# Optimization experiments

Hardware: AMD Instinct MI355X
Metric: run time of the kernel (lower is better)

The kernel has to match this reference:

```python
import jax, jax.numpy as jnp
import numpy as np
from jax import lax

INIT_STRIDE = 10.0
COARSE_STRIDE = 4.0
DOWN_SAMPLE = 4.0
NUM_POINT = 128
N_INST = 2000


def setup_inputs() -> dict:
    key = jax.random.key(0)
    ks = jax.random.split(key, 12)
    B, C, H, W = 4, 64, 256, 256
    return {
        'cnn_feature': jax.random.normal(ks[0], (B, C, H, W), jnp.float32),
        'wh_pred': jax.random.normal(ks[1], (B, NUM_POINT * 2, H, W), jnp.float32),
        'ct_ind': jax.random.randint(ks[2], (N_INST,), 0, H * W, jnp.int64 if jax.config.jax_enable_x64 else jnp.int32),
        'ct_img_idx': jax.random.randint(ks[3], (N_INST,), 0, B, jnp.int64 if jax.config.jax_enable_x64 else jnp.int32),
        'conv1_w': jax.random.normal(ks[4], (256, 64, 3, 3), jnp.float32) * 0.05,
        'conv1_b': jax.random.normal(ks[5], (256,), jnp.float32) * 0.05,
        'conv2_w': jax.random.normal(ks[6], (64, 256, 1, 1), jnp.float32) * 0.05,
        'conv2_b': jax.random.normal(ks[7], (64,), jnp.float32) * 0.05,
        'w_poly': jax.random.normal(ks[8], (NUM_POINT * 4, (NUM_POINT + 1) * 64), jnp.float32) * 0.02,
        'w_fuse': jax.random.normal(ks[9], (NUM_POINT * 2, NUM_POINT * 4), jnp.float32) * 0.02,
        'b_fuse': jax.random.normal(ks[10], (NUM_POINT * 2,), jnp.float32) * 0.02,
    }


def bilinear_sample(feat, pts, img_idx):
    # feat [B,C,H,W]; pts [N,P,2] pixel coords; img_idx [N]
    # matches torch grid_sample(align_corners=False, padding_mode='zeros')
    # with grid = pts/(WH/2) - 1  =>  sample coord = pts - 0.5
    B, C, H, W = feat.shape
    sx = pts[..., 0] - 0.5
    sy = pts[..., 1] - 0.5
    x0 = jnp.floor(sx).astype(jnp.int32); x1 = x0 + 1
    y0 = jnp.floor(sy).astype(jnp.int32); y1 = y0 + 1
    wx1 = sx - x0; wx0 = 1.0 - wx1
    wy1 = sy - y0; wy0 = 1.0 - wy1
    bidx = img_idx[:, None].astype(jnp.int32)  # [N,1]

    def corner(yc, xc, w):
        valid = (xc >= 0) & (xc < W) & (yc >= 0) & (yc < H)
        g = feat[bidx, :, jnp.clip(yc, 0, H - 1), jnp.clip(xc, 0, W - 1)]  # [N,P,C]
        return g * (w * valid)[..., None]

    out = (corner(y0, x0, wy0 * wx0) + corner(y0, x1, wy0 * wx1)
           + corner(y1, x0, wy1 * wx0) + corner(y1, x1, wy1 * wx1))
    return out  # [N,P,C]


def _forward(cnn_feature, wh_pred, ct_ind, ct_img_idx, conv1_w, conv1_b, conv2_w, conv2_b, w_poly, w_fuse, b_fuse):
    B, Cf, H, W = cnn_feature.shape
    N = ct_ind.shape[0]
    ct_x = jnp.clip(ct_ind % W, 0, W - 1)
    ct_y = jnp.clip(ct_ind // W, 0, H - 1)
    # gather polygon offsets at center locations: [N, 2*P] -> [N, P, 2]
    ct_offset = wh_pred[ct_img_idx, :, ct_y, ct_x].reshape(N, NUM_POINT, 2)
    ct = jnp.stack([ct_x, ct_y], axis=1).astype(jnp.float32)  # [N,2]
    init_polys = ct_offset * INIT_STRIDE + ct[:, None, :]  # [N,P,2]

    # Refine.trans_feature: conv3x3(64->256)+ReLU -> conv1x1(256->64)
    dn = ('NCHW', 'OIHW', 'NCHW')
    f = lax.conv_general_dilated(cnn_feature, conv1_w, (1, 1), 'SAME', dimension_numbers=dn) + conv1_b[None, :, None, None]
    f = jax.nn.relu(f)
    f = lax.conv_general_dilated(f, conv2_w, (1, 1), 'VALID', dimension_numbers=dn) + conv2_b[None, :, None, None]

    points = jnp.concatenate([ct[:, None, :], init_polys], axis=1)  # [N,P+1,2]
    fp = bilinear_sample(f, points, ct_img_idx)  # [N,P+1,64]
    fp = fp.transpose(0, 2, 1).reshape(N, -1)  # [N, 64*(P+1)] (C-major like torch)

    off = fp @ w_poly.T            # trans_poly (no bias)
    off = off @ w_fuse.T + b_fuse  # trans_fuse
    off = off.reshape(N, NUM_POINT, 2)
    coarse_polys = off * COARSE_STRIDE + lax.stop_gradient(init_polys)
    # stacked outputs: poly_init*down, poly_coarse*down -> [2,N,P,2]
    return jnp.stack([init_polys * DOWN_SAMPLE, coarse_polys * DOWN_SAMPLE])


def reference(cnn_feature, wh_pred, ct_ind, ct_img_idx, conv1_w, conv1_b, conv2_w, conv2_b, w_poly, w_fuse, b_fuse):
    return _forward(cnn_feature, wh_pred, ct_ind, ct_img_idx, conv1_w, conv1_b, conv2_w, conv2_b, w_poly, w_fuse, b_fuse)
```

## Files before the change

kernel.cpp:

```cpp
#include <hip/hip_runtime.h>

typedef unsigned short ushort_t;
typedef __bf16 bf16x8 __attribute__((ext_vector_type(8)));
typedef float f32x4 __attribute__((ext_vector_type(4)));

__device__ __forceinline__ ushort_t f2b(float f) {
  union { float f; unsigned u; } v; v.f = f;
  unsigned r = v.u + 0x7FFFu + ((v.u >> 16) & 1u);
  return (ushort_t)(r >> 16);
}
__device__ __forceinline__ float b2f(ushort_t u) {
  union { unsigned u; float f; } v; v.u = ((unsigned)u) << 16;
  return v.f;
}
__device__ __forceinline__ f32x4 MFMA(bf16x8 a, bf16x8 b, f32x4 c) {
  return __builtin_amdgcn_mfma_f32_16x16x32_bf16(a, b, c, 0, 0, 0);
}
__device__ __forceinline__ void gload_lds16(const ushort_t* g, ushort_t* l) {
  __builtin_amdgcn_global_load_lds(
      (const __attribute__((address_space(1))) unsigned int*)g,
      (__attribute__((address_space(3))) unsigned int*)l, 16, 0, 0);
}

#define XTW 258

__global__ void zero_border_kernel(ushort_t* __restrict__ xt) {
  int i = blockIdx.x * 256 + threadIdx.x;
  if (i >= 32896) return;
  int px_id = i >> 3, oct = (i & 7) << 3;
  int img = px_id / 1028, r = px_id - img * 1028;
  int row, col;
  if (r < 516) { row = (r < 258) ? 0 : 257; col = (r < 258) ? r : r - 258; }
  else { int rr = r - 516; row = 1 + (rr >> 1); col = (rr & 1) ? 257 : 0; }
  uint4 z = make_uint4(0, 0, 0, 0);
  *(uint4*)(xt + (((size_t)img * XTW + row) * XTW + col) * 64 + oct) = z;
}

__global__ void cast_xt_kernel(const float* __restrict__ x, ushort_t* __restrict__ xt) {
  __shared__ float tile[64][65];
  int blk = blockIdx.x;
  int b = blk >> 10, rest = blk & 1023;
  int y = rest >> 2, xseg = (rest & 3) << 6;
  int p0 = y * 256 + xseg;
  int t = threadIdx.x;
#pragma unroll
  for (int rep = 0; rep < 16; ++rep) {
    int lin = rep * 256 + t;
    int c = lin >> 6, p = lin & 63;
    tile[c][p] = x[((size_t)(b * 64 + c)) * 65536 + p0 + p];
  }
  __syncthreads();
#pragma unroll
  for (int rep = 0; rep < 2; ++rep) {
    int u = rep * 256 + t;
    int p = u >> 3, cc = (u & 7) << 3;
    union { ushort_t s[8]; uint4 v; } pk;
#pragma unroll
    for (int j = 0; j < 8; ++j) pk.s[j] = f2b(tile[cc + j][p]);
    int gx = xseg + p + 1;
    size_t base = (((size_t)b * XTW + (y + 1)) * XTW + gx) * 64;
    *(uint4*)(xt + base + (cc ^ ((gx & 7) << 3))) = pk.v;
  }
}

__global__ void cast_w1t_kernel(const float* __restrict__ w1, ushort_t* __restrict__ w1t2) {
  int i = blockIdx.x * 256 + threadIdx.x;
  int tap = i / 16384;
  int rem = i & 16383;
  int nn = rem >> 6, c = rem & 63;
  int g = nn >> 4, l15v = nn & 15;
  int kk = c >> 5, lg = (c >> 3) & 3, j = c & 7;
  int lanev = lg * 16 + l15v;
  w1t2[((tap * 2 + kk) * 16 + g) * 512 + lanev * 8 + j] = f2b(w1[(nn * 64 + c) * 9 + tap]);
}

__global__ void cast_f32_bf16_kernel(const float* __restrict__ src, ushort_t* __restrict__ dst, int n) {
  for (int i = blockIdx.x * blockDim.x + threadIdx.x; i < n; i += gridDim.x * blockDim.x)
    dst[i] = f2b(src[i]);
}

__global__ void cast_wp_kernel(const float* __restrict__ src, ushort_t* __restrict__ dst) {
  for (int i = blockIdx.x * blockDim.x + threadIdx.x; i < 4227072; i += gridDim.x * blockDim.x) {
    int row = i / 8256;
    int col = i - row * 8256;
    dst[row * 8256 + (col ^ ((row & 7) << 3))] = f2b(src[i]);
  }
}

__global__ void prep_kernel(const float* __restrict__ wh, const int* __restrict__ ct_ind,
                            const int* __restrict__ ct_b, float* __restrict__ out,
                            float* __restrict__ pts) {
  int n = blockIdx.x, t = threadIdx.x;
  int ci = ct_ind[n];
  int b = ct_b[n];
  int ctx = ci & 255;
  int cty = (ci >> 8) & 255;
  float fx = (float)ctx, fy = (float)cty;
  size_t base = ((size_t)b * 256 + 2 * t) * 65536 + (size_t)cty * 256 + ctx;
  float ox = wh[base];
  float oy = wh[base + 65536];
  float ix = ox * 10.f + fx, iy = oy * 10.f + fy;
  out[(n * 128 + t) * 2]     = ix * 4.f;
  out[(n * 128 + t) * 2 + 1] = iy * 4.f;
  float* pn = pts + (size_t)n * 258;
  if (t == 0) { pn[0] = fx; pn[1] = fy; }
  pn[2 + t * 2] = ix;
  pn[3 + t * 2] = iy;
}

__global__ __launch_bounds__(512, 2)
void conv_fused_kernel(const ushort_t* __restrict__ xt, const ushort_t* __restrict__ w1t2,
                       const float* __restrict__ b1, const float* __restrict__ w2,
                       const float* __restrict__ b2, ushort_t* __restrict__ f2) {
  __shared__ __align__(16) char smem[163840];
  ushort_t* strip = (ushort_t*)smem;
  ushort_t* F1    = (ushort_t*)smem;
  ushort_t* W2l   = (ushort_t*)(smem + 131072);
  ushort_t* T     = (ushort_t*)smem;

  int rawblk = blockIdx.x;
  int blk = ((rawblk & 7) << 7) + (rawblk >> 3);
  int b = blk >> 8;
  int rest = blk & 255;
  int y2 = (rest >> 1) << 1;
  int x0 = (rest & 1) << 7;
  int tid = threadIdx.x;
  int wid = tid >> 6, lane = tid & 63;
  int l15 = lane & 15, lg = lane >> 4;
  int wm = (wid >> 1) << 6;
  int wn = (wid & 1) << 7;
  int g0 = wn >> 4;

  for (int c = wid; c < 68; c += 8) {
    int ry = c / 17, ck = c - ry * 17;
    const ushort_t* g = xt + (((size_t)b * XTW + (y2 + ry)) * XTW + x0 + ck * 8) * 64 + lane * 8;
    gload_lds16(g, strip + (ry * 136 + ck * 8) * 64);
  }
  bf16x8 Breg[2][8];
#pragma unroll
  for (int nf = 0; nf < 8; ++nf)
    Breg[0][nf] = *(const bf16x8*)(w1t2 + (size_t)(g0 + nf) * 512 + lane * 8);
  __syncthreads();

  f32x4 acc[4][8] = {};

#pragma unroll
  for (int s = 0; s < 18; ++s) {
    const int tap = s >> 1, kk = s & 1;
    const int cur = s & 1;
    if (s < 17) {
#pragma unroll
      for (int nf = 0; nf < 8; ++nf)
        Breg[cur ^ 1][nf] = *(const bf16x8*)(w1t2 + (size_t)((s + 1) * 16 + g0 + nf) * 512 + lane * 8);
    }
    const int dy = tap / 3 - 1, dx = tap % 3 - 1;
    const int sr  = (wm >> 7) + dy + 1;
    const int spb = (wm & 127) + dx + 1;
    const int c0 = (kk << 5) + (lg << 3);
    bf16x8 a[4];
#pragma unroll
    for (int m = 0; m < 4; ++m) {
      int sp = spb + m * 16 + l15;
      a[m] = *(const bf16x8*)(strip + ((sr * 136 + sp) << 6) + (c0 ^ ((sp & 7) << 3)));
    }
#pragma unroll
    for (int nf = 0; nf < 8; ++nf)
#pragma unroll
      for (int m = 0; m < 4; ++m)
        acc[m][nf] = MFMA(a[m], Breg[cur][nf], acc[m][nf]);
  }
  __syncthreads();

#pragma unroll
  for (int nf = 0; nf < 8; ++nf) {
    int ch = wn + nf * 16 + l15;
    float bias = b1[ch];
#pragma unroll
    for (int m = 0; m < 4; ++m) {
#pragma unroll
      for (int r = 0; r < 4; ++r) {
        int p = wm + m * 16 + lg * 4 + r;
        F1[(p << 8) + (ch ^ ((p & 7) << 3))] = f2b(fmaxf(acc[m][nf][r] + bias, 0.f));
      }
    }
  }
#pragma unroll
  for (int it = 0; it < 4; ++it) {
    int u = it * 512 + tid;
    int oc = u >> 5, ic = (u & 31) << 3;
    float4 fa = *(const float4*)(w2 + (oc << 8) + ic);
    float4 fb = *(const float4*)(w2 + (oc << 8) + ic + 4);
    union { ushort_t s[8]; uint4 v; } pk;
    pk.s[0] = f2b(fa.x); pk.s[1] = f2b(fa.y); pk.s[2] = f2b(fa.z); pk.s[3] = f2b(fa.w);
    pk.s[4] = f2b(fb.x); pk.s[5] = f2b(fb.y); pk.s[6] = f2b(fb.z); pk.s[7] = f2b(fb.w);
    *(uint4*)(W2l + (oc << 8) + (ic ^ ((oc & 7) << 3))) = pk.v;
  }
  __syncthreads();
  int wpx = wid << 5;
  f32x4 acc2[2][4] = {};
#pragma unroll
  for (int kc = 0; kc < 8; ++kc) {
    int c0 = (kc << 5) + (lg << 3);
    bf16x8 a2[2];
#pragma unroll
    for (int mm = 0; mm < 2; ++mm) {
      int p = wpx + mm * 16 + l15;
      a2[mm] = *(const bf16x8*)(F1 + (p << 8) + (c0 ^ ((p & 7) << 3)));
    }
#pragma unroll
    for (int nf = 0; nf < 4; ++nf) {
      int oc = nf * 16 + l15;
      bf16x8 bw = *(const bf16x8*)(W2l + (oc << 8) + (c0 ^ ((oc & 7) << 3)));
#pragma unroll
      for (int mm = 0; mm < 2; ++mm)
        acc2[mm][nf] = MFMA(a2[mm], bw, acc2[mm][nf]);
    }
  }
  __syncthreads();
#pragma unroll
  for (int mm = 0; mm < 2; ++mm)
#pragma unroll
    for (int nf = 0; nf < 4; ++nf) {
      int oc = nf * 16 + l15;
      float bias = b2[oc];
#pragma unroll
      for (int r = 0; r < 4; ++r) {
        int p = wpx + mm * 16 + lg * 4 + r;
        T[(p << 6) + (oc ^ ((p & 7) << 3))] = f2b(acc2[mm][nf][r] + bias);
      }
    }
  __syncthreads();
  const size_t imgbase = (size_t)b * 65536;
#pragma unroll
  for (int it = 0; it < 4; ++it) {
    int u = it * 512 + tid;
    int p = u >> 3, co = (u & 7) << 3;
    uint4 v = *(const uint4*)(T + (p << 6) + (co ^ ((p & 7) << 3)));
    int gpx = (y2 + (p >> 7)) * 256 + x0 + (p & 127);
    *(uint4*)(f2 + (imgbase + gpx) * 64 + co) = v;
  }
}

__global__ void sample_kernel(const ushort_t* __restrict__ f2, const float* __restrict__ pts,
                              const int* __restrict__ ct_b, ushort_t* __restrict__ fp) {
  int n = blockIdx.x, t = threadIdx.x;
  __shared__ float pl[258];
  __shared__ __align__(16) ushort_t fpl[8256];
  int b = ct_b[n];
  const ushort_t* fb = f2 + (size_t)b * 4194304;
  for (int i = t; i < 258; i += 128) pl[i] = pts[(size_t)n * 258 + i];
  __syncthreads();
  int c4 = t & 15;
  int ps = t >> 4;
  for (int base = 0; base < 136; base += 8) {
    int pt = base + ps;
    bool live = pt < 129;
    int ptc = live ? pt : 0;
    float px = pl[ptc * 2], py = pl[ptc * 2 + 1];
    float sx = px - 0.5f, sy = py - 0.5f;
    float fx0 = floorf(sx), fy0 = floorf(sy);
    int x0 = (int)fx0, y0 = (int)fy0;
    float wx1 = sx - fx0, wy1 = sy - fy0;
    float wx0 = 1.f - wx1, wy0 = 1.f - wy1;
    float a0 = 0.f, a1 = 0.f, a2 = 0.f, a3 = 0.f;
#pragma unroll
    for (int cy = 0; cy < 2; ++cy) {
#pragma unroll
      for (int cx = 0; cx < 2; ++cx) {
        int yc = y0 + cy, xc = x0 + cx;
        float w = (cy ? wy1 : wy0) * (cx ? wx1 : wx0);
        bool valid = (xc >= 0) && (xc < 256) && (yc >= 0) && (yc < 256);
        int ycc = min(max(yc, 0), 255), xcc = min(max(xc, 0), 255);
        uint2 v = *(const uint2*)(fb + ((size_t)(ycc * 256 + xcc)) * 64 + (c4 << 2));
        float ww = valid ? w : 0.f;
        a0 += b2f((ushort_t)(v.x & 0xFFFF)) * ww;
        a1 += b2f((ushort_t)(v.x >> 16)) * ww;
        a2 += b2f((ushort_t)(v.y & 0xFFFF)) * ww;
        a3 += b2f((ushort_t)(v.y >> 16)) * ww;
      }
    }
    if (live) {
      int ch = c4 << 2;
      fpl[(ch + 0) * 129 + pt] = f2b(a0);
      fpl[(ch + 1) * 129 + pt] = f2b(a1);
      fpl[(ch + 2) * 129 + pt] = f2b(a2);
      fpl[(ch + 3) * 129 + pt] = f2b(a3);
    }
  }
  __syncthreads();
  uint4* fo = (uint4*)(fp + (size_t)n * 8256);
  const uint4* fi = (const uint4*)fpl;
  int key = n & 7;
  for (int i = t; i < 1032; i += 128) fo[i ^ key] = fi[i];
}

__global__ __launch_bounds__(256)
void gemm_splitk_kernel(const ushort_t* __restrict__ A, const ushort_t* __restrict__ B,
                        float* __restrict__ partials) {
  __shared__ __align__(16) ushort_t Al[8192];
  __shared__ __align__(16) ushort_t Bl[8192];
  int spatial = blockIdx.x;
  int kc = blockIdx.y;
  int n_t = (spatial & 7) >> 1;
  int m_t = ((spatial >> 3) << 1) | (spatial & 1);
  int m0 = m_t << 7, n0 = n_t << 7;
  int ks0 = (129 * kc) >> 3, ks1 = (129 * (kc + 1)) >> 3;

  int tid = threadIdx.x;
  int wid = tid >> 6, lane = tid & 63;
  int l15 = lane & 15, lg = lane >> 4;
  int wm = (wid >> 1) << 6, wn = (wid & 1) << 6;
  int srow = (lane >> 3);
  int soct = lane & 7;
  f32x4 acc[4][4] = {};
  for (int ks = ks0; ks < ks1; ++ks) {
    __syncthreads();
#pragma unroll
    for (int j = 0; j < 4; ++j) {
      int q = (wid << 2) + j;
      int r = (q << 3) + srow;
      int ar = m0 + r;
      if (ar >= 2000) ar = 1992 + (ar & 7);
      gload_lds16(A + (size_t)ar * 8256 + ks * 64 + soct * 8, Al + q * 512);
      gload_lds16(B + (size_t)(n0 + r) * 8256 + ks * 64 + soct * 8, Bl + q * 512);
    }
    __syncthreads();
#pragma unroll
    for (int kk = 0; kk < 2; ++kk) {
      int c0 = (kk << 5) + (lg << 3);
      bf16x8 a[4], b[4];
#pragma unroll
      for (int m = 0; m < 4; ++m) {
        int row = wm + m * 16 + l15;
        a[m] = *(const bf16x8*)(Al + (row << 6) + (c0 ^ ((row & 7) << 3)));
      }
#pragma unroll
      for (int nf = 0; nf < 4; ++nf) {
        int row = wn + nf * 16 + l15;
        b[nf] = *(const bf16x8*)(Bl + (row << 6) + (c0 ^ ((row & 7) << 3)));
      }
#pragma unroll
      for (int m = 0; m < 4; ++m)
#pragma unroll
        for (int nf = 0; nf < 4; ++nf)
          acc[m][nf] = MFMA(a[m], b[nf], acc[m][nf]);
    }
  }
  float* pout = partials + (size_t)kc * 1048576;
#pragma unroll
  for (int m = 0; m < 4; ++m)
#pragma unroll
    for (int nf = 0; nf < 4; ++nf)
#pragma unroll
      for (int r = 0; r < 4; ++r) {
        int row = m0 + wm + m * 16 + lg * 4 + r;
        int col = n0 + wn + nf * 16 + l15;
        pout[(size_t)row * 512 + col] = acc[m][nf][r];
      }
}

__global__ void reduce_splitk_kernel(const float* __restrict__ partials,
                                     ushort_t* __restrict__ off1) {
  int i = blockIdx.x * 256 + threadIdx.x;
  size_t idx = (size_t)i * 4;
  float4 s = *(const float4*)(partials + idx);
#pragma unroll
  for (int c = 1; c < 8; ++c) {
    float4 p = *(const float4*)(partials + (size_t)c * 1048576 + idx);
    s.x += p.x; s.y += p.y; s.z += p.z; s.w += p.w;
  }
  union { ushort_t u[4]; uint2 v; } pk;
  pk.u[0] = f2b(s.x); pk.u[1] = f2b(s.y); pk.u[2] = f2b(s.z); pk.u[3] = f2b(s.w);
  *(uint2*)(off1 + idx) = pk.v;
}

__global__ __launch_bounds__(256)
void gemm64_epi_kernel(const ushort_t* __restrict__ A, const ushort_t* __restrict__ B,
                       const float* __restrict__ bias, const float* __restrict__ out0,
                       float* __restrict__ out1, int Mvalid) {
  __shared__ ushort_t Alds[64][72];
  __shared__ ushort_t Blds[64][72];
  const int K = 512;
  int n0 = blockIdx.x * 64, m0 = blockIdx.y * 64;
  int tid = threadIdx.x;
  int wid = tid >> 6, lane = tid & 63;
  int l15 = lane & 15, lg = lane >> 4;
  int wm = (wid >> 1) * 32, wn = (wid & 1) * 32;
  f32x4 acc[2][2] = {};
  for (int ks = 0; ks < K / 64; ++ks) {
    __syncthreads();
#pragma unroll
    for (int it = 0; it < 2; ++it) {
      int u = it * 256 + tid;
      int r = u >> 3, cc = (u & 7) << 3;
      *(uint4*)(&Alds[r][cc]) = *(const uint4*)(A + (size_t)(m0 + r) * K + ks * 64 + cc);
      *(uint4*)(&Blds[r][cc]) = *(const uint4*)(B + (size_t)(n0 + r) * K + ks * 64 + cc);
    }
    __syncthreads();
#pragma unroll
    for (int kk = 0; kk < 2; ++kk) {
      int c0 = (kk << 5) + (lg << 3);
      bf16x8 a[2], b[2];
      a[0] = *(const bf16x8*)(&Alds[wm + l15][c0]);
      a[1] = *(const bf16x8*)(&Alds[wm + 16 + l15][c0]);
      b[0] = *(const bf16x8*)(&Blds[wn + l15][c0]);
      b[1] = *(const bf16x8*)(&Blds[wn + 16 + l15][c0]);
#pragma unroll
      for (int m = 0; m < 2; ++m)
#pragma unroll
        for (int nf = 0; nf < 2; ++nf)
          acc[m][nf] = MFMA(a[m], b[nf], acc[m][nf]);
    }
  }
#pragma unroll
  for (int m = 0; m < 2; ++m)
#pragma unroll
    for (int nf = 0; nf < 2; ++nf)
#pragma unroll
      for (int r = 0; r < 4; ++r) {
        int row = m0 + wm + m * 16 + lg * 4 + r;
        int col = n0 + wn + nf * 16 + l15;
        if (row < Mvalid) {
          float v = acc[m][nf][r] + bias[col];
          out1[(size_t)row * 256 + col] = v * 16.f + out0[(size_t)row * 256 + col];
        }
      }
}

extern "C" void kernel_launch(void* const* d_in, const int* in_sizes, int n_in,
                              void* d_out, int out_size, void* d_ws, size_t ws_size,
                              hipStream_t stream) {
  const float* x    = (const float*)d_in[0];
  const float* wh   = (const float*)d_in[1];
  const int* ct_ind = (const int*)d_in[2];
  const int* ct_b   = (const int*)d_in[3];
  const float* w1   = (const float*)d_in[4];
  const float* b1   = (const float*)d_in[5];
  const float* w2   = (const float*)d_in[6];
  const float* b2   = (const float*)d_in[7];
  const float* wp   = (const float*)d_in[8];
  const float* wf   = (const float*)d_in[9];
  const float* bfu  = (const float*)d_in[10];
  float* out = (float*)d_out;
  char* ws = (char*)d_ws;

  ushort_t* xt    = (ushort_t*)(ws + 0);
  float* partials = (float*)(ws + 0);
  ushort_t* w1t2  = (ushort_t*)(ws + 34080768);
  ushort_t* f2    = (ushort_t*)(ws + 34375680);
  ushort_t* wpb   = (ushort_t*)(ws + 67930112);
  ushort_t* wfb   = (ushort_t*)(ws + 76384256);
  ushort_t* fp    = (ushort_t*)(ws + 76646400);
  ushort_t* off1  = (ushort_t*)(ws + 109670400);
  float*    pts   = (float*)(ws + 111767552);

  zero_border_kernel<<<dim3(129), dim3(256), 0, stream>>>(xt);
  cast_xt_kernel<<<dim3(4096), dim3(256), 0, stream>>>(x, xt);
  cast_w1t_kernel<<<dim3(576), dim3(256), 0, stream>>>(w1, w1t2);
  cast_wp_kernel<<<dim3(2064), dim3(256), 0, stream>>>(wp, wpb);
  cast_f32_bf16_kernel<<<dim3(64), dim3(256), 0, stream>>>(wf, wfb, 131072);
  prep_kernel<<<dim3(2000), dim3(128), 0, stream>>>(wh, ct_ind, ct_b, out, pts);
  conv_fused_kernel<<<dim3(1024), dim3(512), 0, stream>>>(xt, w1t2, b1, w2, b2, f2);
  sample_kernel<<<dim3(2000), dim3(128), 0, stream>>>(f2, pts, ct_b, fp);
  gemm_splitk_kernel<<<dim3(64, 8), dim3(256), 0, stream>>>(fp, wpb, partials);
  reduce_splitk_kernel<<<dim3(1024), dim3(256), 0, stream>>>(partials, off1);
  gemm64_epi_kernel<<<dim3(4, 32), dim3(256), 0, stream>>>(off1, wfb, bfu, out,
                                                           out + 512000, 2000);
}
```

Before: 224.2 us.

## Fuse input NCHW-to-bf16 transpose and zero padding into conv kernel

```diff
diff --git a/kernel.cpp b/kernel.cpp
--- a/kernel.cpp
+++ b/kernel.cpp
@@ -20,47 +20,6 @@
   __builtin_amdgcn_global_load_lds(
       (const __attribute__((address_space(1))) unsigned int*)g,
       (__attribute__((address_space(3))) unsigned int*)l, 16, 0, 0);
-}
-
-#define XTW 258
-
-__global__ void zero_border_kernel(ushort_t* __restrict__ xt) {
-  int i = blockIdx.x * 256 + threadIdx.x;
-  if (i >= 32896) return;
-  int px_id = i >> 3, oct = (i & 7) << 3;
-  int img = px_id / 1028, r = px_id - img * 1028;
-  int row, col;
-  if (r < 516) { row = (r < 258) ? 0 : 257; col = (r < 258) ? r : r - 258; }
-  else { int rr = r - 516; row = 1 + (rr >> 1); col = (rr & 1) ? 257 : 0; }
-  uint4 z = make_uint4(0, 0, 0, 0);
-  *(uint4*)(xt + (((size_t)img * XTW + row) * XTW + col) * 64 + oct) = z;
-}
-
-__global__ void cast_xt_kernel(const float* __restrict__ x, ushort_t* __restrict__ xt) {
-  __shared__ float tile[64][65];
-  int blk = blockIdx.x;
-  int b = blk >> 10, rest = blk & 1023;
-  int y = rest >> 2, xseg = (rest & 3) << 6;
-  int p0 = y * 256 + xseg;
-  int t = threadIdx.x;
-#pragma unroll
-  for (int rep = 0; rep < 16; ++rep) {
-    int lin = rep * 256 + t;
-    int c = lin >> 6, p = lin & 63;
-    tile[c][p] = x[((size_t)(b * 64 + c)) * 65536 + p0 + p];
-  }
-  __syncthreads();
-#pragma unroll
-  for (int rep = 0; rep < 2; ++rep) {
-    int u = rep * 256 + t;
-    int p = u >> 3, cc = (u & 7) << 3;
-    union { ushort_t s[8]; uint4 v; } pk;
-#pragma unroll
-    for (int j = 0; j < 8; ++j) pk.s[j] = f2b(tile[cc + j][p]);
-    int gx = xseg + p + 1;
-    size_t base = (((size_t)b * XTW + (y + 1)) * XTW + gx) * 64;
-    *(uint4*)(xt + base + (cc ^ ((gx & 7) << 3))) = pk.v;
-  }
 }
 
 __global__ void cast_w1t_kernel(const float* __restrict__ w1, ushort_t* __restrict__ w1t2) {
@@ -109,11 +68,12 @@
 }
 
 __global__ __launch_bounds__(512, 2)
-void conv_fused_kernel(const ushort_t* __restrict__ xt, const ushort_t* __restrict__ w1t2,
+void conv_fused_kernel(const float* __restrict__ x, const ushort_t* __restrict__ w1t2,
                        const float* __restrict__ b1, const float* __restrict__ w2,
                        const float* __restrict__ b2, ushort_t* __restrict__ f2) {
   __shared__ __align__(16) char smem[163840];
   ushort_t* strip = (ushort_t*)smem;
+  float*    tile2 = (float*)(smem + 69632);
   ushort_t* F1    = (ushort_t*)smem;
   ushort_t* W2l   = (ushort_t*)(smem + 131072);
   ushort_t* T     = (ushort_t*)smem;
@@ -131,16 +91,45 @@
   int wn = (wid & 1) << 7;
   int g0 = wn >> 4;
 
-  for (int c = wid; c < 68; c += 8) {
-    int ry = c / 17, ck = c - ry * 17;
-    const ushort_t* g = xt + (((size_t)b * XTW + (y2 + ry)) * XTW + x0 + ck * 8) * 64 + lane * 8;
-    gload_lds16(g, strip + (ry * 136 + ck * 8) * 64);
-  }
   bf16x8 Breg[2][8];
 #pragma unroll
   for (int nf = 0; nf < 8; ++nf)
     Breg[0][nf] = *(const bf16x8*)(w1t2 + (size_t)(g0 + nf) * 512 + lane * 8);
-  __syncthreads();
+
+  const float* xb = x + (size_t)b * 4194304;
+#pragma unroll
+  for (int st = 0; st < 2; ++st) {
+#pragma unroll
+    for (int it = 0; it < 34; ++it) {
+      int u = it * 512 + tid;
+      int rr = u / 8704;
+      int rem = u - rr * 8704;
+      int c = rem / 136, tp = rem - c * 136;
+      int ys = y2 + st * 2 + rr - 1;
+      int xs = x0 + tp - 1;
+      float v = 0.f;
+      if (ys >= 0 && ys < 256 && xs >= 0 && xs < 256)
+        v = xb[(size_t)c * 65536 + ys * 256 + xs];
+      tile2[(rr * 64 + c) * 137 + tp] = v;
+    }
+    __syncthreads();
+#pragma unroll
+    for (int it = 0; it < 5; ++it) {
+      int u = it * 512 + tid;
+      if (u < 2176) {
+        int rr = u / 1088;
+        int rem = u - rr * 1088;
+        int tp = rem >> 3, oc = rem & 7;
+        union { ushort_t s[8]; uint4 v4; } pk;
+#pragma unroll
+        for (int j = 0; j < 8; ++j)
+          pk.s[j] = f2b(tile2[(rr * 64 + oc * 8 + j) * 137 + tp]);
+        int ry = st * 2 + rr;
+        *(uint4*)(strip + ((ry * 136 + tp) << 6) + ((oc << 3) ^ ((tp & 7) << 3))) = pk.v4;
+      }
+    }
+    __syncthreads();
+  }
 
   f32x4 acc[4][8] = {};
 
@@ -444,7 +433,6 @@
   float* out = (float*)d_out;
   char* ws = (char*)d_ws;
 
-  ushort_t* xt    = (ushort_t*)(ws + 0);
   float* partials = (float*)(ws + 0);
   ushort_t* w1t2  = (ushort_t*)(ws + 34080768);
   ushort_t* f2    = (ushort_t*)(ws + 34375680);
@@ -454,13 +442,11 @@
   ushort_t* off1  = (ushort_t*)(ws + 109670400);
   float*    pts   = (float*)(ws + 111767552);
 
-  zero_border_kernel<<<dim3(129), dim3(256), 0, stream>>>(xt);
-  cast_xt_kernel<<<dim3(4096), dim3(256), 0, stream>>>(x, xt);
   cast_w1t_kernel<<<dim3(576), dim3(256), 0, stream>>>(w1, w1t2);
   cast_wp_kernel<<<dim3(2064), dim3(256), 0, stream>>>(wp, wpb);
   cast_f32_bf16_kernel<<<dim3(64), dim3(256), 0, stream>>>(wf, wfb, 131072);
   prep_kernel<<<dim3(2000), dim3(128), 0, stream>>>(wh, ct_ind, ct_b, out, pts);
-  conv_fused_kernel<<<dim3(1024), dim3(512), 0, stream>>>(xt, w1t2, b1, w2, b2, f2);
+  conv_fused_kernel<<<dim3(1024), dim3(512), 0, stream>>>(x, w1t2, b1, w2, b2, f2);
   sample_kernel<<<dim3(2000), dim3(128), 0, stream>>>(f2, pts, ct_b, fp);
   gemm_splitk_kernel<<<dim3(64, 8), dim3(256), 0, stream>>>(fp, wpb, partials);
   reduce_splitk_kernel<<<dim3(1024), dim3(256), 0, stream>>>(partials, off1);
```

After: 308.5 us. 37.6% more time.
